# Optimization experiments

Measured on AMD Instinct MI355X. Metric: run time of the kernel, lower is better.

The kernel has to match this reference:

```python
import jax, jax.numpy as jnp
import numpy as np

NUM_HEADS = 16

def setup_inputs() -> dict:
    key = jax.random.key(0)
    k0, k1, k2, k3 = jax.random.split(key, 4)
    B, N, Nl, Nr, D = 16, 257, 514, 512, 1024
    gather_idx = jax.random.randint(k0, (B, N), 0, B * Nl + Nr, dtype=jnp.int64 if jax.config.jax_enable_x64 else jnp.int32)
    lhs_states = jax.random.normal(k1, (4, B, Nl, D), dtype=jnp.float32)
    rhs_states = jax.random.normal(k2, (4, 1, Nr, D), dtype=jnp.float32)
    Wo = jax.random.normal(k3, (D, D), dtype=jnp.float32) * 0.02
    bo = jnp.zeros((D,), dtype=jnp.float32)
    return {"gather_idx": gather_idx, "lhs_states": lhs_states, "rhs_states": rhs_states, "Wo": Wo, "bo": bo}


def _gather_stacked_batched_states(gather_idx, lhs_states, rhs_states):
    # lhs_states: [4, B, Nl, D] cache; rhs_states: [4, 1, Nr, D]
    # torch builds batched_states [4, 1, B*Nl+Nr, D] then gathers with [4, B, N, D] idx
    S, B, Nl, D = lhs_states.shape
    Nr = rhs_states.shape[2]
    batched = jnp.concatenate(
        [lhs_states.reshape(S, B * Nl, D), rhs_states.reshape(S, Nr, D)], axis=1
    )  # [4, B*Nl+Nr, D]
    N = gather_idx.shape[1]
    gathered = jnp.take(batched, gather_idx.reshape(-1), axis=1)  # [4, B*N, D]
    return gathered.reshape(S, B, N, D)


def reference(gather_idx, lhs_states, rhs_states, Wo, bo):
    # Gather hidden/q/k/v states from the expanded cache buffer (token reuse dispatch)
    gathered = _gather_stacked_batched_states(gather_idx, lhs_states, rhs_states)
    hidden, q, k, v = gathered[0], gathered[1], gathered[2], gathered[3]
    B, N, D = hidden.shape
    H = NUM_HEADS
    hd = D // H
    scale = hd ** -0.5
    # _shape: [B, N, D] -> [B, H, N, hd]; query scaled before bmm as in torch
    qh = (q * scale).reshape(B, N, H, hd).transpose(0, 2, 1, 3)
    kh = k.reshape(B, N, H, hd).transpose(0, 2, 1, 3)
    vh = v.reshape(B, N, H, hd).transpose(0, 2, 1, 3)
    attn_weights = jax.nn.softmax(jnp.einsum('bhqd,bhkd->bhqk', qh, kh), axis=-1)
    attn_out = jnp.einsum('bhqk,bhkd->bhqd', attn_weights, vh)  # [B, H, N, hd]
    attn_out = attn_out.transpose(0, 2, 1, 3).reshape(B, N, D)
    attn_out = attn_out @ Wo.T + bo  # out_proj (torch Linear)
    return hidden + attn_out  # residual
```

## Files before the change

### kernel.cpp

```cpp
#include <hip/hip_runtime.h>
#include <hip/hip_bf16.h>

typedef __attribute__((ext_vector_type(8))) short bf16x8;
typedef __attribute__((ext_vector_type(4))) float f32x4;
typedef unsigned short u16;
typedef unsigned int u32;

#define LHS_STRIDE 8421376
#define RHS_STRIDE 524288
#define TBL_SPLIT  8224
#define AN 257
#define NR 4112
#define KSD 72
#define VSD 260

__device__ __forceinline__ const float* tbl_row(int s, int g,
    const float* __restrict__ lhs, const float* __restrict__ rhs) {
  if (g < TBL_SPLIT) return lhs + (size_t)s * LHS_STRIDE + (size_t)g * 1024;
  return rhs + (size_t)s * RHS_STRIDE + (size_t)(g - TBL_SPLIT) * 1024;
}

__device__ __forceinline__ u16 f2b(float x) {
  union { __hip_bfloat16 b; u16 u; } c;
  c.b = __float2bfloat16(x);
  return c.u;
}

__device__ __forceinline__ u32 pk2(float a, float b) {
  return (u32)f2b(a) | ((u32)f2b(b) << 16);
}

__device__ __forceinline__ bf16x8 mk8(ushort4 a, ushort4 b) {
  bf16x8 r;
  r[0] = (short)a.x; r[1] = (short)a.y; r[2] = (short)a.z; r[3] = (short)a.w;
  r[4] = (short)b.x; r[5] = (short)b.y; r[6] = (short)b.z; r[7] = (short)b.w;
  return r;
}

__device__ __forceinline__ void gload16(const u16* g, u16* l) {
  __builtin_amdgcn_global_load_lds((const __attribute__((address_space(1))) void*)g,
                                   (__attribute__((address_space(3))) void*)l,
                                   16, 0, 0);
}

__global__ void gather_cvt_kernel(
    const int* __restrict__ gidx, const float* __restrict__ lhs,
    const float* __restrict__ rhs, const float* __restrict__ Wo,
    u16* __restrict__ q_bf, u16* __restrict__ k_bf, u16* __restrict__ v_bf,
    u16* __restrict__ wo_bf) {
  const int blk = blockIdx.x, t = threadIdx.x;
  const float* src;
  u16* dst;
  float sc = 1.0f;
  if (blk < 3 * NR) {
    const int s = blk / NR + 1;
    const int row = blk - (s - 1) * NR;
    src = tbl_row(s, gidx[row], lhs, rhs);
    if (s == 1) { sc = 0.125f; dst = q_bf + (size_t)row * 1024; }
    else if (s == 2) dst = k_bf + (size_t)row * 1024;
    else dst = v_bf + (size_t)row * 1024;
  } else {
    const int row = blk - 3 * NR;
    src = Wo + (size_t)row * 1024;
    dst = wo_bf + (size_t)row * 1024;
  }
  float4 v = *(const float4*)(src + t * 4);
  *(ushort4*)(dst + t * 4) =
      make_ushort4(f2b(sc * v.x), f2b(sc * v.y), f2b(sc * v.z), f2b(sc * v.w));
}

struct __align__(16) AttnSmem {
  u16 K[272 * KSD];
  u16 VT[64 * VSD];
};

__global__ __launch_bounds__(512) void attn_kernel(
    const u16* __restrict__ q_bf, const u16* __restrict__ k_bf,
    const u16* __restrict__ v_bf, u16* __restrict__ attn_out) {
  __shared__ AttnSmem sm;
  const int bh = blockIdx.x, b = bh >> 4, h = bh & 15;
  const int t = threadIdx.x, wave = t >> 6, lane = t & 63;
  const int lg = lane >> 4, lr = lane & 15;
  const u16* qb = q_bf + (size_t)b * AN * 1024 + h * 64;
  const u16* kb = k_bf + (size_t)b * AN * 1024 + h * 64;
  const u16* vb = v_bf + (size_t)b * AN * 1024 + h * 64;

  {
    const int r8 = t >> 3, c8 = (t & 7) * 8;
#pragma unroll
    for (int p = 0; p < 5; ++p) {
      int r = p * 64 + r8;
      if (r < AN) {
        uint4 kx = *(const uint4*)(kb + (size_t)r * 1024 + c8);
        *(uint4*)&sm.K[r * KSD + c8] = kx;
        ushort4 v0 = *(const ushort4*)(vb + (size_t)r * 1024 + c8);
        ushort4 v1 = *(const ushort4*)(vb + (size_t)r * 1024 + c8 + 4);
        sm.VT[(c8 + 0) * VSD + r] = v0.x; sm.VT[(c8 + 1) * VSD + r] = v0.y;
        sm.VT[(c8 + 2) * VSD + r] = v0.z; sm.VT[(c8 + 3) * VSD + r] = v0.w;
        sm.VT[(c8 + 4) * VSD + r] = v1.x; sm.VT[(c8 + 5) * VSD + r] = v1.y;
        sm.VT[(c8 + 6) * VSD + r] = v1.z; sm.VT[(c8 + 7) * VSD + r] = v1.w;
      }
    }
  }

  const int ntile = (wave == 0) ? 3 : 2;
  const int rts[3] = {wave, wave + 8, 16};
  bf16x8 qa[3][2];
#pragma unroll
  for (int ti = 0; ti < 3; ++ti) {
    if (ti < ntile) {
      int qrow = rts[ti] * 16 + lr; if (qrow > 256) qrow = 256;
      const u16* qp = qb + (size_t)qrow * 1024 + lg * 8;
      qa[ti][0] = *(const bf16x8*)qp;
      qa[ti][1] = *(const bf16x8*)(qp + 32);
    }
  }
  __syncthreads();

  const int srcE = lr + ((lane & 16) << 1);
  const int srcO = srcE + 16;
  const bool useE = (lg < 2);

  for (int ti = 0; ti < ntile; ++ti) {
    const int r0 = rts[ti] * 16;

    f32x4 s[17];
#pragma unroll
    for (int nf = 0; nf < 17; ++nf) {
      const u16* kp = &sm.K[(nf * 16 + lr) * KSD + lg * 8];
      ushort4 x0 = *(const ushort4*)kp;
      ushort4 x1 = *(const ushort4*)(kp + 4);
      ushort4 y0 = *(const ushort4*)(kp + 32);
      ushort4 y1 = *(const ushort4*)(kp + 36);
      f32x4 acc = {0.f, 0.f, 0.f, 0.f};
      acc = __builtin_amdgcn_mfma_f32_16x16x32_bf16(mk8(x0, x1), qa[ti][0], acc, 0, 0, 0);
      acc = __builtin_amdgcn_mfma_f32_16x16x32_bf16(mk8(y0, y1), qa[ti][1], acc, 0, 0, 0);
      s[nf] = acc;
    }
    s[16][1] = -1e30f; s[16][2] = -1e30f; s[16][3] = -1e30f;
    if (lg != 0) s[16][0] = -1e30f;

    float m = -1e30f;
#pragma unroll
    for (int nf = 0; nf < 17; ++nf)
      m = fmaxf(m, fmaxf(fmaxf(s[nf][0], s[nf][1]), fmaxf(s[nf][2], s[nf][3])));
    m = fmaxf(m, __shfl_xor(m, 16));
    m = fmaxf(m, __shfl_xor(m, 32));
    float sum = 0.f;
#pragma unroll
    for (int nf = 0; nf < 17; ++nf) {
#pragma unroll
      for (int r = 0; r < 4; ++r) {
        float w = __expf(s[nf][r] - m);
        s[nf][r] = w;
        sum += w;
      }
    }
    sum += __shfl_xor(sum, 16);
    sum += __shfl_xor(sum, 32);
    const float inv = 1.0f / sum;

    f32x4 zero = {0.f, 0.f, 0.f, 0.f};
    f32x4 o[4] = {zero, zero, zero, zero};
#pragma unroll
    for (int ks = 0; ks < 8; ++ks) {
      u32 e0 = pk2(s[2 * ks][0] * inv, s[2 * ks][1] * inv);
      u32 e1 = pk2(s[2 * ks][2] * inv, s[2 * ks][3] * inv);
      u32 f0 = pk2(s[2 * ks + 1][0] * inv, s[2 * ks + 1][1] * inv);
      u32 f1 = pk2(s[2 * ks + 1][2] * inv, s[2 * ks + 1][3] * inv);
      u32 A0 = (u32)__shfl((int)e0, srcE), A1 = (u32)__shfl((int)e1, srcE);
      u32 A2 = (u32)__shfl((int)e0, srcO), A3 = (u32)__shfl((int)e1, srcO);
      u32 B0 = (u32)__shfl((int)f0, srcE), B1 = (u32)__shfl((int)f1, srcE);
      u32 B2 = (u32)__shfl((int)f0, srcO), B3 = (u32)__shfl((int)f1, srcO);
      union { u32 w[4]; bf16x8 v; } pa;
      pa.w[0] = useE ? A0 : B0; pa.w[1] = useE ? A1 : B1;
      pa.w[2] = useE ? A2 : B2; pa.w[3] = useE ? A3 : B3;
#pragma unroll
      for (int nd = 0; nd < 4; ++nd) {
        const u16* vp = &sm.VT[(nd * 16 + lr) * VSD + ks * 32 + lg * 8];
        bf16x8 vbr = mk8(*(const ushort4*)vp, *(const ushort4*)(vp + 4));
        o[nd] = __builtin_amdgcn_mfma_f32_16x16x32_bf16(pa.v, vbr, o[nd], 0, 0, 0);
      }
    }
    {
      union { u32 w[4]; bf16x8 v; } pa;
      pa.w[0] = pk2(s[16][0] * inv, 0.f);
      pa.w[1] = 0; pa.w[2] = 0; pa.w[3] = 0;
#pragma unroll
      for (int nd = 0; nd < 4; ++nd) {
        union { u32 w[4]; bf16x8 v; } vv;
        vv.w[0] = (lg == 0) ? (u32)sm.VT[(nd * 16 + lr) * VSD + 256] : 0u;
        vv.w[1] = 0; vv.w[2] = 0; vv.w[3] = 0;
        o[nd] = __builtin_amdgcn_mfma_f32_16x16x32_bf16(pa.v, vv.v, o[nd], 0, 0, 0);
      }
    }

#pragma unroll
    for (int nd = 0; nd < 4; ++nd)
#pragma unroll
      for (int reg = 0; reg < 4; ++reg) {
        int row = r0 + lg * 4 + reg;
        if (row < AN)
          attn_out[(size_t)(b * AN + row) * 1024 + h * 64 + nd * 16 + lr] =
              f2b(o[nd][reg]);
      }
  }
}

__global__ __launch_bounds__(256, 1) void gemm_kernel(
    const u16* __restrict__ A, const u16* __restrict__ Bw,
    const float* __restrict__ bo, const int* __restrict__ gidx,
    const float* __restrict__ lhs, const float* __restrict__ rhs,
    float* __restrict__ out) {
  __shared__ __align__(16) u16 As[2][128 * 32];
  __shared__ __align__(16) u16 Bs[2][128 * 32];
  const int t = threadIdx.x, wave = t >> 6, lane = t & 63;
  const int lg = lane >> 4, lr = lane & 15;
  const int linear = (blockIdx.x & 7) * 33 + (blockIdx.x >> 3);
  const int mt = linear >> 3, nt = linear & 7;
  const int m0 = mt * 128, n0 = nt * 128;
  const int wm = wave >> 1, wn = wave & 1;

  f32x4 zero = {0.f, 0.f, 0.f, 0.f};
  f32x4 acc[4][4];
#pragma unroll
  for (int i = 0; i < 4; ++i)
#pragma unroll
    for (int j = 0; j < 4; ++j) acc[i][j] = zero;

  const int srow = lane >> 2;
  const int scol = (((lane & 3) ^ ((lane >> 3) & 3))) * 8;
  const int ss = (lg ^ ((lr >> 1) & 3)) * 8;

#define STAGE(buf, kt)                                                          \
  {                                                                             \
    const int k0 = (kt) * 32;                                                   \
    _Pragma("unroll")                                                           \
    for (int i = 0; i < 2; ++i) {                                               \
      int row = wave * 32 + i * 16 + srow;                                      \
      int arow = m0 + row; if (arow > 4111) arow = 4111;                        \
      gload16(A + (size_t)arow * 1024 + k0 + scol, &As[buf][wave * 1024 + i * 512]); \
      gload16(Bw + (size_t)(n0 + row) * 1024 + k0 + scol, &Bs[buf][wave * 1024 + i * 512]); \
    }                                                                           \
  }

  STAGE(0, 0)
  __syncthreads();
  int cur = 0;
  for (int kt = 0; kt < 32; ++kt) {
    if (kt < 31) STAGE(cur ^ 1, kt + 1)
    bf16x8 af[4], bfr[4];
#pragma unroll
    for (int i = 0; i < 4; ++i) {
      af[i]  = *(const bf16x8*)&As[cur][(wm * 64 + i * 16 + lr) * 32 + ss];
      bfr[i] = *(const bf16x8*)&Bs[cur][(wn * 64 + i * 16 + lr) * 32 + ss];
    }
#pragma unroll
    for (int i = 0; i < 4; ++i)
#pragma unroll
      for (int j = 0; j < 4; ++j)
        acc[i][j] = __builtin_amdgcn_mfma_f32_16x16x32_bf16(af[i], bfr[j], acc[i][j], 0, 0, 0);
    __syncthreads();
    cur ^= 1;
  }
#undef STAGE

#pragma unroll
  for (int i = 0; i < 4; ++i)
#pragma unroll
    for (int j = 0; j < 4; ++j)
#pragma unroll
      for (int reg = 0; reg < 4; ++reg) {
        int row = m0 + wm * 64 + i * 16 + lg * 4 + reg;
        int col = n0 + wn * 64 + j * 16 + lr;
        if (row < 4112) {
          int g = gidx[row];
          out[(size_t)row * 1024 + col] =
              tbl_row(0, g, lhs, rhs)[col] + bo[col] + acc[i][j][reg];
        }
      }
}

extern "C" void kernel_launch(void* const* d_in, const int* in_sizes, int n_in,
                              void* d_out, int out_size, void* d_ws, size_t ws_size,
                              hipStream_t stream) {
  const int*   gidx = (const int*)d_in[0];
  const float* lhs  = (const float*)d_in[1];
  const float* rhs  = (const float*)d_in[2];
  const float* Wo   = (const float*)d_in[3];
  const float* bo   = (const float*)d_in[4];
  float* out = (float*)d_out;

  u16* q_bf    = (u16*)d_ws;
  u16* k_bf    = q_bf + (size_t)NR * 1024;
  u16* v_bf    = k_bf + (size_t)NR * 1024;
  u16* attn_ws = v_bf + (size_t)NR * 1024;
  u16* wo_bf   = attn_ws + (size_t)NR * 1024;

  gather_cvt_kernel<<<3 * NR + 1024, 256, 0, stream>>>(gidx, lhs, rhs, Wo,
                                                       q_bf, k_bf, v_bf, wo_bf);
  attn_kernel<<<256, 512, 0, stream>>>(q_bf, k_bf, v_bf, attn_ws);
  gemm_kernel<<<264, 256, 0, stream>>>(attn_ws, wo_bf, bo, gidx, lhs, rhs, out);
}
```

Measured before the change: 316.4 us.

## Split attention query tiles across two blocks and shrink GEMM tiles to 64x64

The attention kernel now launches two blocks per (batch, head), each handling half of the query row tiles. This doubles the block count from 256 to 512 so all CUs on the device get work. The output-projection GEMM moves from 128x128 tiles with double-buffered K=32 stages to 64x64 tiles with single-buffered K=64 stages, giving 1040 blocks instead of 264 and dropping the one-block-per-CU bound. The cost is that K/V are staged twice per head, and the GEMM loses load/compute overlap and gets less data reuse per tile.

```diff
diff --git a/kernel.cpp b/kernel.cpp
--- a/kernel.cpp
+++ b/kernel.cpp
@@ -78,7 +78,8 @@
     const u16* __restrict__ q_bf, const u16* __restrict__ k_bf,
     const u16* __restrict__ v_bf, u16* __restrict__ attn_out) {
   __shared__ AttnSmem sm;
-  const int bh = blockIdx.x, b = bh >> 4, h = bh & 15;
+  const int bh = blockIdx.x >> 1, half = blockIdx.x & 1;
+  const int b = bh >> 4, h = bh & 15;
   const int t = threadIdx.x, wave = t >> 6, lane = t & 63;
   const int lg = lane >> 4, lr = lane & 15;
   const u16* qb = q_bf + (size_t)b * AN * 1024 + h * 64;
@@ -103,11 +104,13 @@
     }
   }
 
-  const int ntile = (wave == 0) ? 3 : 2;
-  const int rts[3] = {wave, wave + 8, 16};
-  bf16x8 qa[3][2];
-#pragma unroll
-  for (int ti = 0; ti < 3; ++ti) {
+  int rts[2];
+  int ntile;
+  if (half == 0) { rts[0] = wave; rts[1] = 16; ntile = (wave == 0) ? 2 : 1; }
+  else           { rts[0] = wave + 8; rts[1] = 0; ntile = 1; }
+  bf16x8 qa[2][2];
+#pragma unroll
+  for (int ti = 0; ti < 2; ++ti) {
     if (ti < ntile) {
       int qrow = rts[ti] * 16 + lr; if (qrow > 256) qrow = 256;
       const u16* qp = qb + (size_t)qrow * 1024 + lg * 8;
@@ -207,72 +210,71 @@
   }
 }
 
-__global__ __launch_bounds__(256, 1) void gemm_kernel(
+__global__ __launch_bounds__(256) void gemm_kernel(
     const u16* __restrict__ A, const u16* __restrict__ Bw,
     const float* __restrict__ bo, const int* __restrict__ gidx,
     const float* __restrict__ lhs, const float* __restrict__ rhs,
     float* __restrict__ out) {
-  __shared__ __align__(16) u16 As[2][128 * 32];
-  __shared__ __align__(16) u16 Bs[2][128 * 32];
+  __shared__ __align__(16) u16 As[64 * 64];
+  __shared__ __align__(16) u16 Bs[64 * 64];
   const int t = threadIdx.x, wave = t >> 6, lane = t & 63;
   const int lg = lane >> 4, lr = lane & 15;
-  const int linear = (blockIdx.x & 7) * 33 + (blockIdx.x >> 3);
-  const int mt = linear >> 3, nt = linear & 7;
-  const int m0 = mt * 128, n0 = nt * 128;
+  const int linear = (blockIdx.x & 7) * 130 + (blockIdx.x >> 3);
+  const int mt = linear >> 4, nt = linear & 15;
+  const int m0 = mt * 64, n0 = nt * 64;
   const int wm = wave >> 1, wn = wave & 1;
 
   f32x4 zero = {0.f, 0.f, 0.f, 0.f};
-  f32x4 acc[4][4];
-#pragma unroll
-  for (int i = 0; i < 4; ++i)
-#pragma unroll
-    for (int j = 0; j < 4; ++j) acc[i][j] = zero;
-
-  const int srow = lane >> 2;
-  const int scol = (((lane & 3) ^ ((lane >> 3) & 3))) * 8;
-  const int ss = (lg ^ ((lr >> 1) & 3)) * 8;
-
-#define STAGE(buf, kt)                                                          \
-  {                                                                             \
-    const int k0 = (kt) * 32;                                                   \
-    _Pragma("unroll")                                                           \
-    for (int i = 0; i < 2; ++i) {                                               \
-      int row = wave * 32 + i * 16 + srow;                                      \
-      int arow = m0 + row; if (arow > 4111) arow = 4111;                        \
-      gload16(A + (size_t)arow * 1024 + k0 + scol, &As[buf][wave * 1024 + i * 512]); \
-      gload16(Bw + (size_t)(n0 + row) * 1024 + k0 + scol, &Bs[buf][wave * 1024 + i * 512]); \
-    }                                                                           \
-  }
-
-  STAGE(0, 0)
-  __syncthreads();
-  int cur = 0;
-  for (int kt = 0; kt < 32; ++kt) {
-    if (kt < 31) STAGE(cur ^ 1, kt + 1)
-    bf16x8 af[4], bfr[4];
-#pragma unroll
-    for (int i = 0; i < 4; ++i) {
-      af[i]  = *(const bf16x8*)&As[cur][(wm * 64 + i * 16 + lr) * 32 + ss];
-      bfr[i] = *(const bf16x8*)&Bs[cur][(wn * 64 + i * 16 + lr) * 32 + ss];
-    }
-#pragma unroll
-    for (int i = 0; i < 4; ++i)
-#pragma unroll
-      for (int j = 0; j < 4; ++j)
-        acc[i][j] = __builtin_amdgcn_mfma_f32_16x16x32_bf16(af[i], bfr[j], acc[i][j], 0, 0, 0);
+  f32x4 acc[2][2];
+#pragma unroll
+  for (int i = 0; i < 2; ++i)
+#pragma unroll
+    for (int j = 0; j < 2; ++j) acc[i][j] = zero;
+
+  const int trow0 = t >> 3, slot0 = t & 7;
+  const int scg0 = (slot0 ^ (trow0 & 7)) * 8;
+  const int arow0 = (m0 + trow0 > 4111) ? 4111 : m0 + trow0;
+  const int trow1 = trow0 + 32, slot1 = slot0;
+  const int scg1 = (slot1 ^ (trow1 & 7)) * 8;
+  const int arow1 = (m0 + trow1 > 4111) ? 4111 : m0 + trow1;
+  const int rs0 = ((0 * 4 + lg) ^ (lr & 7)) * 8;
+  const int rs1 = ((1 * 4 + lg) ^ (lr & 7)) * 8;
+
+  for (int kt = 0; kt < 16; ++kt) {
+    const int k0 = kt * 64;
+    gload16(A + (size_t)arow0 * 1024 + k0 + scg0, &As[(t & ~63) * 8]);
+    gload16(A + (size_t)arow1 * 1024 + k0 + scg1, &As[2048 + (t & ~63) * 8]);
+    gload16(Bw + (size_t)(n0 + trow0) * 1024 + k0 + scg0, &Bs[(t & ~63) * 8]);
+    gload16(Bw + (size_t)(n0 + trow1) * 1024 + k0 + scg1, &Bs[2048 + (t & ~63) * 8]);
     __syncthreads();
-    cur ^= 1;
-  }
-#undef STAGE
-
-#pragma unroll
-  for (int i = 0; i < 4; ++i)
-#pragma unroll
-    for (int j = 0; j < 4; ++j)
+    bf16x8 af[2][2], bfr[2][2];
+#pragma unroll
+    for (int i = 0; i < 2; ++i) {
+      int ra = wm * 32 + i * 16 + lr;
+      int rb = wn * 32 + i * 16 + lr;
+      af[i][0]  = *(const bf16x8*)&As[ra * 64 + rs0];
+      af[i][1]  = *(const bf16x8*)&As[ra * 64 + rs1];
+      bfr[i][0] = *(const bf16x8*)&Bs[rb * 64 + rs0];
+      bfr[i][1] = *(const bf16x8*)&Bs[rb * 64 + rs1];
+    }
+#pragma unroll
+    for (int i = 0; i < 2; ++i)
+#pragma unroll
+      for (int j = 0; j < 2; ++j) {
+        acc[i][j] = __builtin_amdgcn_mfma_f32_16x16x32_bf16(af[i][0], bfr[j][0], acc[i][j], 0, 0, 0);
+        acc[i][j] = __builtin_amdgcn_mfma_f32_16x16x32_bf16(af[i][1], bfr[j][1], acc[i][j], 0, 0, 0);
+      }
+    __syncthreads();
+  }
+
+#pragma unroll
+  for (int i = 0; i < 2; ++i)
+#pragma unroll
+    for (int j = 0; j < 2; ++j)
 #pragma unroll
       for (int reg = 0; reg < 4; ++reg) {
-        int row = m0 + wm * 64 + i * 16 + lg * 4 + reg;
-        int col = n0 + wn * 64 + j * 16 + lr;
+        int row = m0 + wm * 32 + i * 16 + lg * 4 + reg;
+        int col = n0 + wn * 32 + j * 16 + lr;
         if (row < 4112) {
           int g = gidx[row];
           out[(size_t)row * 1024 + col] =
@@ -299,6 +301,6 @@
 
   gather_cvt_kernel<<<3 * NR + 1024, 256, 0, stream>>>(gidx, lhs, rhs, Wo,
                                                        q_bf, k_bf, v_bf, wo_bf);
-  attn_kernel<<<256, 512, 0, stream>>>(q_bf, k_bf, v_bf, attn_ws);
-  gemm_kernel<<<264, 256, 0, stream>>>(attn_ws, wo_bf, bo, gidx, lhs, rhs, out);
-}
+  attn_kernel<<<512, 512, 0, stream>>>(q_bf, k_bf, v_bf, attn_ws);
+  gemm_kernel<<<1040, 256, 0, stream>>>(attn_ws, wo_bf, bo, gidx, lhs, rhs, out);
+}
```

New measurement: 291.1 us. 1.09x faster.
